# Kernel optimization log

Measured on AMD Instinct MI355X. Metric: run time of the kernel, lower is better.

## Reference

```python
import jax, jax.numpy as jnp
import numpy as np

N, E, T, F = 20000, 320000, 64, 16
HG, HT = 128, 256


def setup_inputs() -> dict:
    key = jax.random.key(0)
    ks = jax.random.split(key, 18)
    s = 0.05
    p = lambda k, shape: jax.random.normal(k, shape, jnp.float32) * s
    return {
        "x_seq": jax.random.normal(ks[0], (1, T, N, F), jnp.float32),
        "edge_index": jax.random.randint(ks[1], (2, E), 0, N, jnp.int32),
        # SAGEConv 1 (PyG default: mean aggregation; lin_l on aggregated neighbors w/ bias, lin_r on root w/o bias)
        "W1l": p(ks[2], (HG, F)), "b1l": p(ks[3], (HG,)), "W1r": p(ks[4], (HG, F)),
        # SAGEConv 2
        "W2l": p(ks[5], (HG, HG)), "b2l": p(ks[6], (HG,)), "W2r": p(ks[7], (HG, HG)),
        # GRU (torch gate order: r, z, n)
        "W_ih": p(ks[8], (3 * HT, HG)), "W_hh": p(ks[9], (3 * HT, HT)),
        "b_ih": p(ks[10], (3 * HT,)), "b_hh": p(ks[11], (3 * HT,)),
        # head: Linear(HT,64) -> ReLU -> Linear(64,1)
        "Wh1": p(ks[12], (64, HT)), "bh1": p(ks[13], (64,)),
        "Wh2": p(ks[14], (1, 64)), "bh2": p(ks[15], (1,)),
    }


def reference(x_seq, edge_index, W1l, b1l, W1r, W2l, b2l, W2r,
              W_ih, W_hh, b_ih, b_hh, Wh1, bh1, Wh2, bh2):
    n_nodes = x_seq.shape[2]
    src, dst = edge_index[0], edge_index[1]
    # in-degree for mean aggregation (0 -> output 0, matching scatter-mean)
    deg = jax.ops.segment_sum(jnp.ones(src.shape[0], x_seq.dtype), dst,
                              num_segments=n_nodes)
    inv_deg = jnp.where(deg > 0, 1.0 / deg, 0.0)[:, None]  # [N,1]

    def sage(x, Wl, bl, Wr):
        # mean over incoming neighbor messages, then linear + root linear
        agg = jax.ops.segment_sum(x[src], dst, num_segments=n_nodes) * inv_deg
        return agg @ Wl.T + bl + x @ Wr.T

    def graph_step(carry, x_t):  # x_t: [N, F]
        h = jax.nn.relu(sage(x_t, W1l, b1l, W1r))
        h = jax.nn.relu(sage(h, W2l, b2l, W2r))
        return carry, h.mean(axis=0)  # [HG]

    _, Hg = jax.lax.scan(graph_step, 0, x_seq[0])  # [T, HG]

    hidden_t = W_hh.shape[1]

    def gru_step(h, x_t):
        gi = x_t @ W_ih.T + b_ih
        gh = h @ W_hh.T + b_hh
        i_r, i_z, i_n = jnp.split(gi, 3)
        h_r, h_z, h_n = jnp.split(gh, 3)
        r = jax.nn.sigmoid(i_r + h_r)
        z = jax.nn.sigmoid(i_z + h_z)
        n = jnp.tanh(i_n + r * h_n)
        h_new = (1.0 - z) * n + z * h
        return h_new, h_new

    h0 = jnp.zeros((hidden_t,), x_seq.dtype)
    h_last, _ = jax.lax.scan(gru_step, h0, Hg)  # [HT]

    y = jax.nn.relu(h_last @ Wh1.T + bh1) @ Wh2.T + bh2  # [1]
    return y
```

## Files before the change

### kernel.cpp

```cpp
#include <hip/hip_runtime.h>
#include <hip/hip_bf16.h>

#define N_NODES 20000
#define N_EDGES 320000
#define T_STEPS 64
#define F_IN    16
#define HGd     128
#define HTd     256
#define INVN    (1.0f/20000.0f)
#define NTILES   625
#define S1T      79
#define NG64     313
#define QSCALE   64.0f
#define INVQ     (1.0f/64.0f)
#define QX       32.0f
#define INVQX    (1.0f/32.0f)

typedef __attribute__((ext_vector_type(8))) short short8;
typedef __attribute__((ext_vector_type(4))) float f32x4;
typedef __attribute__((ext_vector_type(2))) float f32x2;
typedef __attribute__((ext_vector_type(2))) _Float16 half2t;

static __device__ __forceinline__ ushort f2bf(float f) {
    __hip_bfloat16 b = __float2bfloat16(f);
    return *reinterpret_cast<ushort*>(&b);
}
static __device__ __forceinline__ half2t u2h(uint u) {
    half2t h; __builtin_memcpy(&h, &u, 4); return h;
}
static __device__ __forceinline__ uint packf16(float a, float b) {
    auto h = __builtin_amdgcn_cvt_pkrtz(a, b);
    uint u; __builtin_memcpy(&u, &h, 4); return u;
}

__global__ void k_zero(int* __restrict__ deg, float* __restrict__ HgP,
                       int* __restrict__ cnt, int* __restrict__ jobc,
                       int* __restrict__ bins) {
    int i = blockIdx.x * blockDim.x + threadIdx.x;
    if (i < N_NODES) deg[i] = 0;
    if (i < T_STEPS * 8 * HGd) HgP[i] = 0.0f;
    if (i < 2) cnt[i] = 0;
    if (i < 1024) jobc[i] = 0;
    if (i < 256) bins[i] = 0;
}

__global__ void k_degree(const int* __restrict__ ei, int* __restrict__ deg) {
    int e = blockIdx.x * blockDim.x + threadIdx.x;
    if (e < N_EDGES) atomicAdd(&deg[ei[N_EDGES + e]], 1);
}

__global__ __launch_bounds__(1024) void k_scan(const int* __restrict__ deg,
        int* __restrict__ rp, int* __restrict__ cursor, float* __restrict__ invd) {
    __shared__ int sh[1024];
    __shared__ int carry_s;
    int tid = threadIdx.x;
    if (tid == 0) { carry_s = 0; rp[0] = 0; }
    __syncthreads();
    for (int base = 0; base < N_NODES; base += 1024) {
        int i = base + tid;
        int v = (i < N_NODES) ? deg[i] : 0;
        sh[tid] = v;
        __syncthreads();
        for (int off = 1; off < 1024; off <<= 1) {
            int t = (tid >= off) ? sh[tid - off] : 0;
            __syncthreads();
            sh[tid] += t;
            __syncthreads();
        }
        int inc = sh[tid] + carry_s;
        if (i < N_NODES) {
            rp[i + 1] = inc;
            cursor[i] = inc - v;
            invd[i] = (v > 0) ? (1.0f / (float)v) : 0.0f;
        }
        __syncthreads();
        if (tid == 1023) carry_s = inc;
        __syncthreads();
    }
}

__global__ void k_fill(const int* __restrict__ ei, int* __restrict__ cursor,
                       int* __restrict__ csr) {
    int e = blockIdx.x * blockDim.x + threadIdx.x;
    if (e < N_EDGES) {
        int d = ei[N_EDGES + e];
        int p = atomicAdd(&cursor[d], 1);
        csr[p] = ei[e];
    }
}

__global__ void k_hist(const int* __restrict__ deg, int* __restrict__ bins) {
    int i = blockIdx.x * blockDim.x + threadIdx.x;
    if (i < N_NODES) atomicAdd(&bins[min(deg[i], 255)], 1);
}

__global__ __launch_bounds__(256) void k_binscan(const int* __restrict__ bins,
        int* __restrict__ bincur, int* __restrict__ nodebefore, int* __restrict__ edgebefore) {
    __shared__ int sh[256], she[256];
    int tid = threadIdx.x;
    int b = bins[tid];
    sh[tid] = b;
    she[tid] = b * tid;
    __syncthreads();
    for (int off = 1; off < 256; off <<= 1) {
        int v = (tid >= off) ? sh[tid - off] : 0;
        int ve = (tid >= off) ? she[tid - off] : 0;
        __syncthreads();
        sh[tid] += v; she[tid] += ve;
        __syncthreads();
    }
    bincur[tid] = sh[tid] - b;
    nodebefore[tid] = sh[tid] - b;
    edgebefore[tid] = she[tid] - b * tid;
}

__global__ void k_perm(const int* __restrict__ deg, int* __restrict__ bincur,
                       const int* __restrict__ nodebefore, const int* __restrict__ edgebefore,
                       const float* __restrict__ invd,
                       int* __restrict__ perm, int* __restrict__ pos,
                       int* __restrict__ rp2, float* __restrict__ invd2,
                       int* __restrict__ degs2) {
    int i = blockIdx.x * blockDim.x + threadIdx.x;
    if (i < N_NODES) {
        int d = min(deg[i], 255);
        int p = atomicAdd(&bincur[d], 1);
        int rank = p - nodebefore[d];
        perm[p] = i;
        pos[i] = p;
        rp2[p] = edgebefore[d] + rank * d;
        invd2[p] = invd[i];
        degs2[p] = deg[i];
        if (i == 0) rp2[N_NODES] = N_EDGES;
    }
}

__global__ void k_csr2(const int* __restrict__ rp, const int* __restrict__ pos,
                       const int* __restrict__ rp2, const int* __restrict__ csr,
                       int* __restrict__ csr2) {
    int i = blockIdx.x * blockDim.x + threadIdx.x;
    if (i < N_NODES) {
        int s = rp[i], e = rp[i + 1];
        int o = rp2[pos[i]];
        for (int k = s; k < e; ++k) csr2[o + (k - s)] = csr[k];
    }
}

__global__ __launch_bounds__(512) void k_tb(const int* __restrict__ rp2, int* __restrict__ tb) {
    __shared__ int sh[512];
    int t = threadIdx.x;
    int md = 0;
    if (t < NG64 && t * 64 < N_NODES) {
        int last = min((t + 1) * 64, N_NODES) - 1;
        md = rp2[last + 1] - rp2[last];
    }
    sh[t] = 64 * md;
    __syncthreads();
    for (int off = 1; off < 512; off <<= 1) {
        int v = (t >= off) ? sh[t - off] : 0;
        __syncthreads();
        sh[t] += v;
        __syncthreads();
    }
    tb[t + 1] = sh[t];
    if (t == 0) tb[0] = 0;
}

__global__ void k_csr3(const int* __restrict__ rp2, const int* __restrict__ tb,
                       const int* __restrict__ csr2, int* __restrict__ csr3) {
    int p = blockIdx.x * blockDim.x + threadIdx.x;
    if (p < N_NODES) {
        int s = rp2[p], d = rp2[p + 1] - s;
        int base = tb[p >> 6];
        int lane = p & 63;
        for (int j = 0; j < d; ++j) csr3[base + j * 64 + lane] = csr2[s + j];
    }
}

__global__ void k_qx(const float* __restrict__ xs, int* __restrict__ x8, int n4) {
    int i = blockIdx.x * blockDim.x + threadIdx.x;
    if (i < n4) {
        float4 v = reinterpret_cast<const float4*>(xs)[i];
        int q8 = __builtin_amdgcn_cvt_pk_fp8_f32(v.x * QX, v.y * QX, 0, false);
        q8 = __builtin_amdgcn_cvt_pk_fp8_f32(v.z * QX, v.w * QX, q8, true);
        x8[i] = q8;
    }
}

__global__ void k_prepw(const float* __restrict__ W1l, const float* __restrict__ W1r,
                        const float* __restrict__ W2l, const float* __restrict__ W2r,
                        const float* __restrict__ W_ih, const float* __restrict__ W_hh,
                        ushort* __restrict__ W1T2, ushort* __restrict__ WT2,
                        float* __restrict__ WihT, uint* __restrict__ W_hhq) {
    int i = blockIdx.x * blockDim.x + threadIdx.x;
    const int n1 = 128 * 32, n2 = 128 * 256, n3 = 128 * 768, n4 = 128 * 768;
    if (i < n1) {
        int o = i >> 5, k = i & 31;
        float v = (k < 16) ? W1l[o * 16 + k] : W1r[o * 16 + (k - 16)];
        W1T2[i] = f2bf(v);
    } else if (i < n1 + n2) {
        int j = i - n1; int o = j >> 8, k = j & 255;
        float v = (k < 128) ? W2l[o * 128 + k] : W2r[o * 128 + (k - 128)];
        WT2[j] = f2bf(v);
    } else if (i < n1 + n2 + n3) {
        int j = i - n1 - n2; int k = j / 768, g = j % 768;
        WihT[j] = W_ih[g * 128 + k];
    } else if (i < n1 + n2 + n3 + n4) {
        int j = i - n1 - n2 - n3; int dw = j / 768, row = j % 768;
        float a = W_hh[(size_t)row * HTd + 2 * dw];
        float b = W_hh[(size_t)row * HTd + 2 * dw + 1];
        W_hhq[j] = packf16(a, b);
    }
}

__global__ __launch_bounds__(256) void k_sage1(
        const char* __restrict__ x8_, const int* __restrict__ tb,
        const int* __restrict__ csr3, const int* __restrict__ degs2,
        const float* __restrict__ invd2,
        const ushort* __restrict__ W1T2, const float* __restrict__ b1l,
        const int* __restrict__ perm, uchar1* __restrict__ h1q_,
        int* __restrict__ jobc, int C) {
    __shared__ ushort u[256 * 40];
    __shared__ int pnode[256];
    __shared__ int job_s;
    int tid = threadIdx.x;
    int l = tid & 63, w = tid >> 6;
    int lane15 = l & 15, g4 = l >> 4;
    const int xcd = blockIdx.x & 7;
    const int cmin = (C < 8) ? C : 8;
    const int ci = xcd % cmin;
    const int reps = (C >= 8) ? (C >> 3) : 1;
    int* ctr = jobc + ci;
    const int njobs = reps * S1T;

    short8 bfr1[2];
    float bb1[2];
#pragma unroll
    for (int ct = 0; ct < 2; ++ct) {
        int o16 = w * 32 + ct * 16 + lane15;
        bfr1[ct] = *reinterpret_cast<const short8*>(W1T2 + o16 * 32 + g4 * 8);
        bb1[ct] = b1l[o16];
    }

    for (;;) {
        if (tid == 0) job_s = atomicAdd(ctr, 1);
        __syncthreads();
        int job = job_s;
        if (job >= njobs) break;
        int rep = job / S1T;
        int tile = job - rep * S1T;
        int tl = ci + (rep << 3);
        const char* xq = x8_ + (size_t)tl * N_NODES * F_IN;
        char* h1q = (char*)h1q_ + (size_t)tl * N_NODES * HGd;
        int p = tile * 256 + tid;
        int node = (p < N_NODES) ? perm[p] : -1;
        pnode[tid] = node;

        float acc[16];
#pragma unroll
        for (int k = 0; k < 16; ++k) acc[k] = 0.0f;
        float rootv[16];
#pragma unroll
        for (int k = 0; k < 16; ++k) rootv[k] = 0.0f;
        if (node >= 0) {
            int d = degs2[p];
            const int base = tb[p >> 6] + (p & 63);
            for (int j = 0; j < d; ++j) {
                int idx = csr3[base + j * 64];
                uint4 row = *reinterpret_cast<const uint4*>(xq + (size_t)idx * F_IN);
#pragma unroll
                for (int c = 0; c < 4; ++c) {
                    uint vd = c == 0 ? row.x : c == 1 ? row.y : c == 2 ? row.z : row.w;
                    f32x2 lo = __builtin_amdgcn_cvt_pk_f32_fp8((int)vd, false);
                    f32x2 hi = __builtin_amdgcn_cvt_pk_f32_fp8((int)vd, true);
                    acc[4 * c + 0] += lo.x; acc[4 * c + 1] += lo.y;
                    acc[4 * c + 2] += hi.x; acc[4 * c + 3] += hi.y;
                }
            }
            float id = invd2[p] * INVQX;
#pragma unroll
            for (int k = 0; k < 16; ++k) acc[k] *= id;
            uint4 rv = *reinterpret_cast<const uint4*>(xq + (size_t)node * F_IN);
#pragma unroll
            for (int c = 0; c < 4; ++c) {
                uint vd = c == 0 ? rv.x : c == 1 ? rv.y : c == 2 ? rv.z : rv.w;
                f32x2 lo = __builtin_amdgcn_cvt_pk_f32_fp8((int)vd, false);
                f32x2 hi = __builtin_amdgcn_cvt_pk_f32_fp8((int)vd, true);
                rootv[4 * c + 0] = lo.x * INVQX; rootv[4 * c + 1] = lo.y * INVQX;
                rootv[4 * c + 2] = hi.x * INVQX; rootv[4 * c + 3] = hi.y * INVQX;
            }
        }
        {
            uint dw[16];
#pragma unroll
            for (int i = 0; i < 8; ++i)
                dw[i] = (uint)f2bf(acc[2 * i]) | ((uint)f2bf(acc[2 * i + 1]) << 16);
#pragma unroll
            for (int i = 0; i < 8; ++i)
                dw[8 + i] = (uint)f2bf(rootv[2 * i]) | ((uint)f2bf(rootv[2 * i + 1]) << 16);
            ushort* ur = u + tid * 40;
#pragma unroll
            for (int c = 0; c < 4; ++c)
                *reinterpret_cast<uint4*>(ur + c * 8) =
                    make_uint4(dw[4 * c], dw[4 * c + 1], dw[4 * c + 2], dw[4 * c + 3]);
        }
        __syncthreads();

#pragma unroll 4
        for (int rt = 0; rt < 16; ++rt) {
            int row = rt * 16 + lane15;
            short8 af = *reinterpret_cast<const short8*>(u + row * 40 + g4 * 8);
            f32x4 a0 = __builtin_amdgcn_mfma_f32_16x16x32_bf16(af, bfr1[0], (f32x4)(0.0f), 0, 0, 0);
            f32x4 a1 = __builtin_amdgcn_mfma_f32_16x16x32_bf16(af, bfr1[1], (f32x4)(0.0f), 0, 0, 0);
#pragma unroll
            for (int j = 0; j < 4; ++j) {
                int nl = rt * 16 + g4 * 4 + j;
                int nd = pnode[nl];
                if (nd >= 0) {
                    float v0 = fmaxf(a0[j] + bb1[0], 0.0f) * QSCALE;
                    float v1 = fmaxf(a1[j] + bb1[1], 0.0f) * QSCALE;
                    int q0 = __builtin_amdgcn_cvt_pk_fp8_f32(v0, v0, 0, false);
                    int q1 = __builtin_amdgcn_cvt_pk_fp8_f32(v1, v1, 0, false);
                    h1q[(size_t)nd * HGd + w * 32 + lane15] = (char)q0;
                    h1q[(size_t)nd * HGd + w * 32 + 16 + lane15] = (char)q1;
                }
            }
        }
    }
}

__global__ __launch_bounds__(256) void k_sage2(
        const uchar1* __restrict__ h1q_,
        const int* __restrict__ rp2, const int* __restrict__ csr2,
        const float* __restrict__ invd2,
        const ushort* __restrict__ WT2, const float* __restrict__ b2l,
        const int* __restrict__ perm, float* __restrict__ HgP,
        int* __restrict__ jobc, int t0, int C) {
    __shared__ uint4 usm4[32 * 512 / 16];
    __shared__ int pnode[32];
    __shared__ int job_s;
    char* ub = (char*)usm4;
    int tid = threadIdx.x;
    int l = tid & 63, w = tid >> 6;
    int lane15 = l & 15, g4 = l >> 4;
    const int xcd = blockIdx.x & 7;
    const int cmin = (C < 8) ? C : 8;
    const int ci = xcd % cmin;
    const int reps = (C >= 8) ? (C >> 3) : 1;
    int* ctr = jobc + ci;
    const int njobs = reps * NTILES;

    short8 bfr[2][8];
    float bb[2];
#pragma unroll
    for (int ct = 0; ct < 2; ++ct) {
        int n = w * 32 + ct * 16 + lane15;
        const ushort* bp = WT2 + n * 256 + g4 * 8;
#pragma unroll
        for (int ks = 0; ks < 8; ++ks)
            bfr[ct][ks] = *reinterpret_cast<const short8*>(bp + ks * 32);
        bb[ct] = b2l[n];
    }

    for (;;) {
        if (tid == 0) job_s = atomicAdd(ctr, 1);
        __syncthreads();
        int job = job_s;
        if (job >= njobs) break;
        int rep = job / NTILES;
        int tile = job - rep * NTILES;
        int tl = ci + ((reps - 1 - rep) << 3);
        int t = t0 + tl;
        const char* h1q = (const char*)h1q_ + (size_t)tl * N_NODES * HGd;
        int nbase = tile * 32;
        if (tid < 32) pnode[tid] = perm[nbase + tid];
        __syncthreads();

        {
            int nl = tid >> 3, seg = tid & 7;
            uint4 v = *reinterpret_cast<const uint4*>(h1q + (size_t)pnode[nl] * HGd + seg * 16);
            uint bw[8];
#pragma unroll
            for (int d = 0; d < 4; ++d) {
                uint vd = d == 0 ? v.x : d == 1 ? v.y : d == 2 ? v.z : v.w;
                f32x2 plo = __builtin_amdgcn_cvt_pk_f32_fp8((int)vd, false);
                f32x2 phi = __builtin_amdgcn_cvt_pk_f32_fp8((int)vd, true);
                bw[2 * d]     = (uint)f2bf(plo.x * INVQ) | ((uint)f2bf(plo.y * INVQ) << 16);
                bw[2 * d + 1] = (uint)f2bf(phi.x * INVQ) | ((uint)f2bf(phi.y * INVQ) << 16);
            }
            int base = nl * 512 + 256 + seg * 32;
            int swz = (nl & 7) << 4;
            *reinterpret_cast<uint4*>(ub + (base ^ swz)) =
                make_uint4(bw[0], bw[1], bw[2], bw[3]);
            *reinterpret_cast<uint4*>(ub + ((base + 16) ^ swz)) =
                make_uint4(bw[4], bw[5], bw[6], bw[7]);
        }

#pragma unroll
        for (int g = 0; g < 2; ++g) {
            int nl = w * 8 + g * 4 + g4;
            int sl = rp2[nbase + nl], el = rp2[nbase + nl + 1];
            float af[8] = {0, 0, 0, 0, 0, 0, 0, 0};
            if (el > sl) {
                int idx[8];
#pragma unroll
                for (int uu = 0; uu < 8; ++uu) idx[uu] = csr2[min(sl + uu, el - 1)];
                for (int j = sl; j < el; j += 8) {
                    uint2 vv[8];
#pragma unroll
                    for (int uu = 0; uu < 8; ++uu)
                        vv[uu] = *reinterpret_cast<const uint2*>(h1q + (size_t)idx[uu] * HGd + lane15 * 8);
                    int jn = j + 8;
#pragma unroll
                    for (int uu = 0; uu < 8; ++uu) idx[uu] = csr2[min(jn + uu, el - 1)];
#pragma unroll
                    for (int uu = 0; uu < 8; ++uu) {
                        uint vx = (j + uu < el) ? vv[uu].x : 0u;
                        uint vy = (j + uu < el) ? vv[uu].y : 0u;
                        f32x2 p0 = __builtin_amdgcn_cvt_pk_f32_fp8((int)vx, false);
                        f32x2 p1 = __builtin_amdgcn_cvt_pk_f32_fp8((int)vx, true);
                        f32x2 p2 = __builtin_amdgcn_cvt_pk_f32_fp8((int)vy, false);
                        f32x2 p3 = __builtin_amdgcn_cvt_pk_f32_fp8((int)vy, true);
                        af[0] += p0.x; af[1] += p0.y; af[2] += p1.x; af[3] += p1.y;
                        af[4] += p2.x; af[5] += p2.y; af[6] += p3.x; af[7] += p3.y;
                    }
                }
            }
            float id = invd2[nbase + nl] * INVQ;
            uint4 pk;
            pk.x = (uint)f2bf(af[0] * id) | ((uint)f2bf(af[1] * id) << 16);
            pk.y = (uint)f2bf(af[2] * id) | ((uint)f2bf(af[3] * id) << 16);
            pk.z = (uint)f2bf(af[4] * id) | ((uint)f2bf(af[5] * id) << 16);
            pk.w = (uint)f2bf(af[6] * id) | ((uint)f2bf(af[7] * id) << 16);
            *reinterpret_cast<uint4*>(ub + ((nl * 512 + lane15 * 16) ^ ((nl & 7) << 4))) = pk;
        }
        __syncthreads();

        f32x4 acc[2][2];
#pragma unroll
        for (int rt = 0; rt < 2; ++rt)
#pragma unroll
            for (int ct = 0; ct < 2; ++ct) acc[rt][ct] = (f32x4)(0.0f);

#pragma unroll
        for (int ks = 0; ks < 8; ++ks) {
#pragma unroll
            for (int rt = 0; rt < 2; ++rt) {
                int row = rt * 16 + lane15;
                int byt = (row * 512 + (ks * 32 + g4 * 8) * 2) ^ ((row & 7) << 4);
                short8 af = *reinterpret_cast<const short8*>(ub + byt);
                acc[rt][0] = __builtin_amdgcn_mfma_f32_16x16x32_bf16(af, bfr[0][ks], acc[rt][0], 0, 0, 0);
                acc[rt][1] = __builtin_amdgcn_mfma_f32_16x16x32_bf16(af, bfr[1][ks], acc[rt][1], 0, 0, 0);
            }
        }

#pragma unroll
        for (int ct = 0; ct < 2; ++ct) {
            float sum = 0.f;
#pragma unroll
            for (int rt = 0; rt < 2; ++rt)
#pragma unroll
                for (int j = 0; j < 4; ++j)
                    sum += fmaxf(acc[rt][ct][j] + bb[ct], 0.f);
            sum += __shfl_xor(sum, 16);
            sum += __shfl_xor(sum, 32);
            if (g4 == 0) {
                int n = w * 32 + ct * 16 + lane15;
                atomicAdd(&HgP[(t * 8 + (job & 7)) * HGd + n], sum);
            }
        }
    }
}

__global__ __launch_bounds__(768) void k_gi(const float* __restrict__ HgP,
        const float* __restrict__ WihT, const float* __restrict__ b_ih,
        float* __restrict__ gi_all) {
    __shared__ float x[HGd];
    int t = blockIdx.x, g = threadIdx.x;
    if (g < HGd) {
        float s = 0.f;
#pragma unroll
        for (int p = 0; p < 8; ++p) s += HgP[(t * 8 + p) * HGd + g];
        x[g] = s * INVN;
    }
    __syncthreads();
    float a = b_ih[g];
    for (int k = 0; k < HGd; ++k) a += WihT[k * 768 + g] * x[k];
    gi_all[t * 768 + g] = a;
}

__global__ __launch_bounds__(768, 3) void k_gru1b(const float* __restrict__ gi_all,
        const uint* __restrict__ W_hhq, const float* __restrict__ b_hh,
        const float* __restrict__ Wh1, const float* __restrict__ bh1,
        const float* __restrict__ Wh2, const float* __restrict__ bh2,
        float* __restrict__ out) {
    int tid = threadIdx.x;
    uint wv[128];
#pragma unroll
    for (int i = 0; i < 128; ++i) wv[i] = W_hhq[i * 768 + tid];
    float bh = b_hh[tid];

    __shared__ float hs[HTd];
    __shared__ uint h2s[HTd / 2];
    __shared__ float gh[3 * HTd];
    if (tid < HTd) hs[tid] = 0.0f;
    if (tid < HTd / 2) h2s[tid] = 0u;
    __syncthreads();

    for (int t = 0; t < T_STEPS; ++t) {
        float s = bh;
#pragma unroll
        for (int i = 0; i < 128; i += 4) {
            uint4 hh = *reinterpret_cast<const uint4*>(&h2s[i]);
            s = __builtin_amdgcn_fdot2(u2h(wv[i + 0]), u2h(hh.x), s, false);
            s = __builtin_amdgcn_fdot2(u2h(wv[i + 1]), u2h(hh.y), s, false);
            s = __builtin_amdgcn_fdot2(u2h(wv[i + 2]), u2h(hh.z), s, false);
            s = __builtin_amdgcn_fdot2(u2h(wv[i + 3]), u2h(hh.w), s, false);
        }
        gh[tid] = s;
        __syncthreads();
        if (tid < HTd) {
            float gir = gi_all[t * 768 + tid];
            float giz = gi_all[t * 768 + HTd + tid];
            float gin = gi_all[t * 768 + 2 * HTd + tid];
            float r = 1.0f / (1.0f + expf(-(gir + gh[tid])));
            float z = 1.0f / (1.0f + expf(-(giz + gh[HTd + tid])));
            float n = tanhf(gin + r * gh[2 * HTd + tid]);
            hs[tid] = (1.0f - z) * n + z * hs[tid];
        }
        __syncthreads();
        if (tid < HTd / 2)
            h2s[tid] = packf16(hs[2 * tid], hs[2 * tid + 1]);
        __syncthreads();
    }

    __shared__ float act[64];
    if (tid < 64) {
        float a = bh1[tid];
        const float* wr = Wh1 + tid * HTd;
        for (int k = 0; k < HTd; k += 4) {
            float4 wv4 = *reinterpret_cast<const float4*>(wr + k);
            a += wv4.x * hs[k] + wv4.y * hs[k + 1] + wv4.z * hs[k + 2] + wv4.w * hs[k + 3];
        }
        act[tid] = fmaxf(a, 0.0f);
    }
    __syncthreads();
    if (tid == 0) {
        float y = bh2[0];
        for (int j = 0; j < 64; ++j) y += Wh2[j] * act[j];
        out[0] = y;
    }
}

extern "C" void kernel_launch(void* const* d_in, const int* in_sizes, int n_in,
                              void* d_out, int out_size, void* d_ws, size_t ws_size,
                              hipStream_t stream) {
    const float* x_seq = (const float*)d_in[0];
    const int*   ei    = (const int*)d_in[1];
    const float* W1l   = (const float*)d_in[2];
    const float* b1l   = (const float*)d_in[3];
    const float* W1r   = (const float*)d_in[4];
    const float* W2l   = (const float*)d_in[5];
    const float* b2l   = (const float*)d_in[6];
    const float* W2r   = (const float*)d_in[7];
    const float* W_ih  = (const float*)d_in[8];
    const float* W_hh  = (const float*)d_in[9];
    const float* b_ih  = (const float*)d_in[10];
    const float* b_hh  = (const float*)d_in[11];
    const float* Wh1   = (const float*)d_in[12];
    const float* bh1   = (const float*)d_in[13];
    const float* Wh2   = (const float*)d_in[14];
    const float* bh2   = (const float*)d_in[15];
    float* out = (float*)d_out;

    char* ws = (char*)d_ws;
    size_t off = 0;
    auto take = [&](size_t nbytes) -> void* {
        void* p = (void*)(ws + off);
        off += (nbytes + 255) & ~(size_t)255;
        return p;
    };
    int*    deg    = (int*)take(N_NODES * 4);
    int*    rp     = (int*)take((N_NODES + 1) * 4);
    int*    cursor = (int*)take(N_NODES * 4);
    int*    csr    = (int*)take(N_EDGES * 4);
    float*  invd   = (float*)take(N_NODES * 4);
    int*    perm   = (int*)take(N_NODES * 4);
    int*    pos    = (int*)take(N_NODES * 4);
    int*    rp2    = (int*)take((N_NODES + 2) * 4);
    int*    csr2   = (int*)take(N_EDGES * 4);
    float*  invd2  = (float*)take(N_NODES * 4);
    int*    degs2  = (int*)take(N_NODES * 4);
    int*    tb     = (int*)take(520 * 4);
    int*    csr3   = (int*)take(360000 * 4);
    int*    bins   = (int*)take(256 * 4);
    int*    bincur = (int*)take(256 * 4);
    int*    nodeb  = (int*)take(256 * 4);
    int*    edgeb  = (int*)take(256 * 4);
    ushort* W1T2   = (ushort*)take(128 * 32 * 2);
    ushort* WT2    = (ushort*)take(128 * 256 * 2);
    float*  WihT   = (float*)take(128 * 768 * 4);
    uint*   W_hhq  = (uint*)take(128 * 768 * 4);
    float*  HgP    = (float*)take(T_STEPS * 8 * HGd * 4);
    float*  gi_all = (float*)take(T_STEPS * 768 * 4);
    int*    cnt    = (int*)take(256);
    int*    jobc   = (int*)take(1024 * 4);

    const size_t slice_q = ((size_t)N_NODES * HGd + 255) & ~(size_t)255;
    const size_t slice_x = ((size_t)N_NODES * F_IN + 255) & ~(size_t)255;
    int T_CH = 64;
    while (T_CH > 1 && off + (size_t)T_CH * (slice_q + slice_x) > ws_size)
        T_CH >>= 1;
    uchar1* h1q = (uchar1*)take((size_t)T_CH * slice_q);
    char*   x8  = (char*)take((size_t)T_CH * slice_x);

    k_zero<<<256, 256, 0, stream>>>(deg, HgP, cnt, jobc, bins);
    k_degree<<<(N_EDGES + 255) / 256, 256, 0, stream>>>(ei, deg);
    k_scan<<<1, 1024, 0, stream>>>(deg, rp, cursor, invd);
    k_fill<<<(N_EDGES + 255) / 256, 256, 0, stream>>>(ei, cursor, csr);
    k_hist<<<(N_NODES + 255) / 256, 256, 0, stream>>>(deg, bins);
    k_binscan<<<1, 256, 0, stream>>>(bins, bincur, nodeb, edgeb);
    k_perm<<<(N_NODES + 255) / 256, 256, 0, stream>>>(deg, bincur, nodeb, edgeb, invd,
                                                      perm, pos, rp2, invd2, degs2);
    k_csr2<<<(N_NODES + 255) / 256, 256, 0, stream>>>(rp, pos, rp2, csr, csr2);
    k_tb<<<1, 512, 0, stream>>>(rp2, tb);
    k_csr3<<<(N_NODES + 255) / 256, 256, 0, stream>>>(rp2, tb, csr2, csr3);
    {
        int total = 128 * 32 + 128 * 256 + 128 * 768 + 128 * 768;
        k_prepw<<<(total + 255) / 256, 256, 0, stream>>>(W1l, W1r, W2l, W2r, W_ih, W_hh,
                                                         W1T2, WT2, WihT, W_hhq);
    }
    int chunk = 0;
    for (int t0 = 0; t0 < T_STEPS; t0 += T_CH, ++chunk) {
        int C = T_CH;
        int n4 = C * N_NODES * F_IN / 4;
        k_qx<<<(n4 + 255) / 256, 256, 0, stream>>>(
            x_seq + (size_t)t0 * N_NODES * F_IN, (int*)x8, n4);
        k_sage1<<<2048, 256, 0, stream>>>(x8, tb, csr3, degs2, invd2, W1T2, b1l, perm,
                                          h1q, jobc + (chunk & 1) * 16, C);
        k_sage2<<<2048, 256, 0, stream>>>(h1q, rp2, csr2, invd2, WT2, b2l, perm, HgP,
                                          jobc + (chunk & 1) * 16 + 8, t0, C);
    }
    k_gi<<<T_STEPS, 768, 0, stream>>>(HgP, WihT, b_ih, gi_all);
    k_gru1b<<<1, 768, 0, stream>>>(gi_all, W_hhq, b_hh, Wh1, bh1, Wh2, bh2, out);
}
```

Baseline: 1.059 ms.

## Store layer-1 activations as fp16 and gather with padded CSR in sage2

```diff
diff --git a/kernel.cpp b/kernel.cpp
--- a/kernel.cpp
+++ b/kernel.cpp
@@ -11,10 +11,9 @@
 #define NTILES   625
 #define S1T      79
 #define NG64     313
-#define QSCALE   64.0f
-#define INVQ     (1.0f/64.0f)
 #define QX       32.0f
 #define INVQX    (1.0f/32.0f)
+#define S_HALF   ((N_NODES + 1) * HGd)
 
 typedef __attribute__((ext_vector_type(8))) short short8;
 typedef __attribute__((ext_vector_type(4))) float f32x4;
@@ -28,20 +27,29 @@
 static __device__ __forceinline__ half2t u2h(uint u) {
     half2t h; __builtin_memcpy(&h, &u, 4); return h;
 }
+static __device__ __forceinline__ uint h2u(half2t h) {
+    uint u; __builtin_memcpy(&u, &h, 4); return u;
+}
 static __device__ __forceinline__ uint packf16(float a, float b) {
     auto h = __builtin_amdgcn_cvt_pkrtz(a, b);
     uint u; __builtin_memcpy(&u, &h, 4); return u;
 }
+static __device__ __forceinline__ ushort f2h(float a) {
+    return (ushort)(packf16(a, a) & 0xffffu);
+}
 
 __global__ void k_zero(int* __restrict__ deg, float* __restrict__ HgP,
-                       int* __restrict__ cnt, int* __restrict__ jobc,
-                       int* __restrict__ bins) {
+                       int* __restrict__ jobc, int* __restrict__ bins,
+                       uint* __restrict__ h1f, int tch) {
     int i = blockIdx.x * blockDim.x + threadIdx.x;
     if (i < N_NODES) deg[i] = 0;
     if (i < T_STEPS * 8 * HGd) HgP[i] = 0.0f;
-    if (i < 2) cnt[i] = 0;
     if (i < 1024) jobc[i] = 0;
     if (i < 256) bins[i] = 0;
+    if (i < tch * 64) {
+        int sl = i >> 6, j = i & 63;
+        h1f[(size_t)sl * (S_HALF / 2) + (size_t)N_NODES * (HGd / 2) + j] = 0u;
+    }
 }
 
 __global__ void k_degree(const int* __restrict__ ei, int* __restrict__ deg) {
@@ -95,31 +103,37 @@
 }
 
 __global__ __launch_bounds__(256) void k_binscan(const int* __restrict__ bins,
-        int* __restrict__ bincur, int* __restrict__ nodebefore, int* __restrict__ edgebefore) {
-    __shared__ int sh[256], she[256];
+        int* __restrict__ bincur, int* __restrict__ nodebefore,
+        int* __restrict__ edgebefore, int* __restrict__ edgebp, int* __restrict__ rp2p) {
+    __shared__ int sh[256], she[256], shp[256];
     int tid = threadIdx.x;
     int b = bins[tid];
+    int dp = (tid + 7) & ~7;
     sh[tid] = b;
     she[tid] = b * tid;
+    shp[tid] = b * dp;
     __syncthreads();
     for (int off = 1; off < 256; off <<= 1) {
         int v = (tid >= off) ? sh[tid - off] : 0;
         int ve = (tid >= off) ? she[tid - off] : 0;
-        __syncthreads();
-        sh[tid] += v; she[tid] += ve;
+        int vp = (tid >= off) ? shp[tid - off] : 0;
+        __syncthreads();
+        sh[tid] += v; she[tid] += ve; shp[tid] += vp;
         __syncthreads();
     }
     bincur[tid] = sh[tid] - b;
     nodebefore[tid] = sh[tid] - b;
     edgebefore[tid] = she[tid] - b * tid;
+    edgebp[tid] = shp[tid] - b * dp;
+    if (tid == 255) rp2p[N_NODES] = shp[255];
 }
 
 __global__ void k_perm(const int* __restrict__ deg, int* __restrict__ bincur,
                        const int* __restrict__ nodebefore, const int* __restrict__ edgebefore,
-                       const float* __restrict__ invd,
+                       const int* __restrict__ edgebp, const float* __restrict__ invd,
                        int* __restrict__ perm, int* __restrict__ pos,
                        int* __restrict__ rp2, float* __restrict__ invd2,
-                       int* __restrict__ degs2) {
+                       int* __restrict__ degs2, int* __restrict__ rp2p) {
     int i = blockIdx.x * blockDim.x + threadIdx.x;
     if (i < N_NODES) {
         int d = min(deg[i], 255);
@@ -128,6 +142,7 @@
         perm[p] = i;
         pos[i] = p;
         rp2[p] = edgebefore[d] + rank * d;
+        rp2p[p] = edgebp[d] + rank * ((d + 7) & ~7);
         invd2[p] = invd[i];
         degs2[p] = deg[i];
         if (i == 0) rp2[N_NODES] = N_EDGES;
@@ -145,6 +160,19 @@
     }
 }
 
+__global__ void k_csr2p(const int* __restrict__ rp, const int* __restrict__ pos,
+                        const int* __restrict__ rp2p, const int* __restrict__ csr,
+                        int* __restrict__ csr2p) {
+    int i = blockIdx.x * blockDim.x + threadIdx.x;
+    if (i < N_NODES) {
+        int s = rp[i], d = rp[i + 1] - s;
+        int dp = (d + 7) & ~7;
+        int o = rp2p[pos[i]];
+        for (int k = 0; k < d; ++k) csr2p[o + k] = csr[s + k];
+        for (int k = d; k < dp; ++k) csr2p[o + k] = N_NODES;
+    }
+}
+
 __global__ __launch_bounds__(512) void k_tb(const int* __restrict__ rp2, int* __restrict__ tb) {
     __shared__ int sh[512];
     int t = threadIdx.x;
@@ -189,7 +217,7 @@
 __global__ void k_prepw(const float* __restrict__ W1l, const float* __restrict__ W1r,
                         const float* __restrict__ W2l, const float* __restrict__ W2r,
                         const float* __restrict__ W_ih, const float* __restrict__ W_hh,
-                        ushort* __restrict__ W1T2, ushort* __restrict__ WT2,
+                        ushort* __restrict__ W1T2, ushort* __restrict__ WT2f,
                         float* __restrict__ WihT, uint* __restrict__ W_hhq) {
     int i = blockIdx.x * blockDim.x + threadIdx.x;
     const int n1 = 128 * 32, n2 = 128 * 256, n3 = 128 * 768, n4 = 128 * 768;
@@ -200,7 +228,7 @@
     } else if (i < n1 + n2) {
         int j = i - n1; int o = j >> 8, k = j & 255;
         float v = (k < 128) ? W2l[o * 128 + k] : W2r[o * 128 + (k - 128)];
-        WT2[j] = f2bf(v);
+        WT2f[j] = f2h(v);
     } else if (i < n1 + n2 + n3) {
         int j = i - n1 - n2; int k = j / 768, g = j % 768;
         WihT[j] = W_ih[g * 128 + k];
@@ -217,7 +245,7 @@
         const int* __restrict__ csr3, const int* __restrict__ degs2,
         const float* __restrict__ invd2,
         const ushort* __restrict__ W1T2, const float* __restrict__ b1l,
-        const int* __restrict__ perm, uchar1* __restrict__ h1q_,
+        const int* __restrict__ perm, ushort* __restrict__ h1f_,
         int* __restrict__ jobc, int C) {
     __shared__ ushort u[256 * 40];
     __shared__ int pnode[256];
@@ -250,7 +278,7 @@
         int tile = job - rep * S1T;
         int tl = ci + (rep << 3);
         const char* xq = x8_ + (size_t)tl * N_NODES * F_IN;
-        char* h1q = (char*)h1q_ + (size_t)tl * N_NODES * HGd;
+        ushort* h1f = h1f_ + (size_t)tl * S_HALF;
         int p = tile * 256 + tid;
         int node = (p < N_NODES) ? perm[p] : -1;
         pnode[tid] = node;
@@ -316,12 +344,10 @@
                 int nl = rt * 16 + g4 * 4 + j;
                 int nd = pnode[nl];
                 if (nd >= 0) {
-                    float v0 = fmaxf(a0[j] + bb1[0], 0.0f) * QSCALE;
-                    float v1 = fmaxf(a1[j] + bb1[1], 0.0f) * QSCALE;
-                    int q0 = __builtin_amdgcn_cvt_pk_fp8_f32(v0, v0, 0, false);
-                    int q1 = __builtin_amdgcn_cvt_pk_fp8_f32(v1, v1, 0, false);
-                    h1q[(size_t)nd * HGd + w * 32 + lane15] = (char)q0;
-                    h1q[(size_t)nd * HGd + w * 32 + 16 + lane15] = (char)q1;
+                    float v0 = fmaxf(a0[j] + bb1[0], 0.0f);
+                    float v1 = fmaxf(a1[j] + bb1[1], 0.0f);
+                    h1f[(size_t)nd * HGd + w * 32 + lane15] = f2h(v0);
+                    h1f[(size_t)nd * HGd + w * 32 + 16 + lane15] = f2h(v1);
                 }
             }
         }
@@ -329,10 +355,10 @@
 }
 
 __global__ __launch_bounds__(256) void k_sage2(
-        const uchar1* __restrict__ h1q_,
-        const int* __restrict__ rp2, const int* __restrict__ csr2,
+        const ushort* __restrict__ h1f_,
+        const int* __restrict__ rp2p, const int* __restrict__ csr2p,
         const float* __restrict__ invd2,
-        const ushort* __restrict__ WT2, const float* __restrict__ b2l,
+        const ushort* __restrict__ WT2f, const float* __restrict__ b2l,
         const int* __restrict__ perm, float* __restrict__ HgP,
         int* __restrict__ jobc, int t0, int C) {
     __shared__ uint4 usm4[32 * 512 / 16];
@@ -354,7 +380,7 @@
 #pragma unroll
     for (int ct = 0; ct < 2; ++ct) {
         int n = w * 32 + ct * 16 + lane15;
-        const ushort* bp = WT2 + n * 256 + g4 * 8;
+        const ushort* bp = WT2f + n * 256 + g4 * 8;
 #pragma unroll
         for (int ks = 0; ks < 8; ++ks)
             bfr[ct][ks] = *reinterpret_cast<const short8*>(bp + ks * 32);
@@ -370,67 +396,53 @@
         int tile = job - rep * NTILES;
         int tl = ci + ((reps - 1 - rep) << 3);
         int t = t0 + tl;
-        const char* h1q = (const char*)h1q_ + (size_t)tl * N_NODES * HGd;
+        const ushort* h1f = h1f_ + (size_t)tl * S_HALF;
         int nbase = tile * 32;
         if (tid < 32) pnode[tid] = perm[nbase + tid];
         __syncthreads();
 
-        {
-            int nl = tid >> 3, seg = tid & 7;
-            uint4 v = *reinterpret_cast<const uint4*>(h1q + (size_t)pnode[nl] * HGd + seg * 16);
-            uint bw[8];
-#pragma unroll
-            for (int d = 0; d < 4; ++d) {
-                uint vd = d == 0 ? v.x : d == 1 ? v.y : d == 2 ? v.z : v.w;
-                f32x2 plo = __builtin_amdgcn_cvt_pk_f32_fp8((int)vd, false);
-                f32x2 phi = __builtin_amdgcn_cvt_pk_f32_fp8((int)vd, true);
-                bw[2 * d]     = (uint)f2bf(plo.x * INVQ) | ((uint)f2bf(plo.y * INVQ) << 16);
-                bw[2 * d + 1] = (uint)f2bf(phi.x * INVQ) | ((uint)f2bf(phi.y * INVQ) << 16);
-            }
-            int base = nl * 512 + 256 + seg * 32;
-            int swz = (nl & 7) << 4;
-            *reinterpret_cast<uint4*>(ub + (base ^ swz)) =
-                make_uint4(bw[0], bw[1], bw[2], bw[3]);
-            *reinterpret_cast<uint4*>(ub + ((base + 16) ^ swz)) =
-                make_uint4(bw[4], bw[5], bw[6], bw[7]);
+        for (int i = tid; i < 512; i += 256) {
+            int nl = i >> 4, seg = i & 15;
+            uint4 v = *reinterpret_cast<const uint4*>(h1f + (size_t)pnode[nl] * HGd + seg * 8);
+            *reinterpret_cast<uint4*>(ub + ((nl * 1024 / 2 + 256 + seg * 16) ^ ((nl & 7) << 4))) = v;
         }
 
 #pragma unroll
         for (int g = 0; g < 2; ++g) {
             int nl = w * 8 + g * 4 + g4;
-            int sl = rp2[nbase + nl], el = rp2[nbase + nl + 1];
-            float af[8] = {0, 0, 0, 0, 0, 0, 0, 0};
-            if (el > sl) {
+            int sl = rp2p[nbase + nl];
+            int dp = rp2p[nbase + nl + 1] - sl;
+            const int* cp = csr2p + sl;
+            half2t a0 = (half2t)0, a1 = (half2t)0, a2 = (half2t)0, a3 = (half2t)0;
+            if (dp > 0) {
                 int idx[8];
 #pragma unroll
-                for (int uu = 0; uu < 8; ++uu) idx[uu] = csr2[min(sl + uu, el - 1)];
-                for (int j = sl; j < el; j += 8) {
-                    uint2 vv[8];
+                for (int uu = 0; uu < 8; ++uu) idx[uu] = cp[uu];
+                for (int j = 0; j < dp; j += 8) {
+                    uint4 vv[8];
 #pragma unroll
                     for (int uu = 0; uu < 8; ++uu)
-                        vv[uu] = *reinterpret_cast<const uint2*>(h1q + (size_t)idx[uu] * HGd + lane15 * 8);
-                    int jn = j + 8;
-#pragma unroll
-                    for (int uu = 0; uu < 8; ++uu) idx[uu] = csr2[min(jn + uu, el - 1)];
+                        vv[uu] = *reinterpret_cast<const uint4*>(h1f + (size_t)idx[uu] * HGd + lane15 * 8);
+                    cp += 8;
+#pragma unroll
+                    for (int uu = 0; uu < 8; ++uu) idx[uu] = cp[uu];
 #pragma unroll
                     for (int uu = 0; uu < 8; ++uu) {
-                        uint vx = (j + uu < el) ? vv[uu].x : 0u;
-                        uint vy = (j + uu < el) ? vv[uu].y : 0u;
-                        f32x2 p0 = __builtin_amdgcn_cvt_pk_f32_fp8((int)vx, false);
-                        f32x2 p1 = __builtin_amdgcn_cvt_pk_f32_fp8((int)vx, true);
-                        f32x2 p2 = __builtin_amdgcn_cvt_pk_f32_fp8((int)vy, false);
-                        f32x2 p3 = __builtin_amdgcn_cvt_pk_f32_fp8((int)vy, true);
-                        af[0] += p0.x; af[1] += p0.y; af[2] += p1.x; af[3] += p1.y;
-                        af[4] += p2.x; af[5] += p2.y; af[6] += p3.x; af[7] += p3.y;
+                        a0 += u2h(vv[uu].x);
+                        a1 += u2h(vv[uu].y);
+                        a2 += u2h(vv[uu].z);
+                        a3 += u2h(vv[uu].w);
                     }
                 }
             }
-            float id = invd2[nbase + nl] * INVQ;
+            float id = invd2[nbase + nl];
+            _Float16 idh = (_Float16)id;
+            half2t idv; idv[0] = idh; idv[1] = idh;
             uint4 pk;
-            pk.x = (uint)f2bf(af[0] * id) | ((uint)f2bf(af[1] * id) << 16);
-            pk.y = (uint)f2bf(af[2] * id) | ((uint)f2bf(af[3] * id) << 16);
-            pk.z = (uint)f2bf(af[4] * id) | ((uint)f2bf(af[5] * id) << 16);
-            pk.w = (uint)f2bf(af[6] * id) | ((uint)f2bf(af[7] * id) << 16);
+            pk.x = h2u(a0 * idv);
+            pk.y = h2u(a1 * idv);
+            pk.z = h2u(a2 * idv);
+            pk.w = h2u(a3 * idv);
             *reinterpret_cast<uint4*>(ub + ((nl * 512 + lane15 * 16) ^ ((nl & 7) << 4))) = pk;
         }
         __syncthreads();
@@ -448,8 +460,8 @@
                 int row = rt * 16 + lane15;
                 int byt = (row * 512 + (ks * 32 + g4 * 8) * 2) ^ ((row & 7) << 4);
                 short8 af = *reinterpret_cast<const short8*>(ub + byt);
-                acc[rt][0] = __builtin_amdgcn_mfma_f32_16x16x32_bf16(af, bfr[0][ks], acc[rt][0], 0, 0, 0);
-                acc[rt][1] = __builtin_amdgcn_mfma_f32_16x16x32_bf16(af, bfr[1][ks], acc[rt][1], 0, 0, 0);
+                acc[rt][0] = __builtin_amdgcn_mfma_f32_16x16x32_f16(af, bfr[0][ks], acc[rt][0], 0, 0, 0);
+                acc[rt][1] = __builtin_amdgcn_mfma_f32_16x16x32_f16(af, bfr[1][ks], acc[rt][1], 0, 0, 0);
             }
         }
 
@@ -587,7 +599,9 @@
     int*    perm   = (int*)take(N_NODES * 4);
     int*    pos    = (int*)take(N_NODES * 4);
     int*    rp2    = (int*)take((N_NODES + 2) * 4);
+    int*    rp2p   = (int*)take((N_NODES + 2) * 4);
     int*    csr2   = (int*)take(N_EDGES * 4);
+    int*    csr2p  = (int*)take(480100 * 4);
     float*  invd2  = (float*)take(N_NODES * 4);
     int*    degs2  = (int*)take(N_NODES * 4);
     int*    tb     = (int*)take(520 * 4);
@@ -596,38 +610,39 @@
     int*    bincur = (int*)take(256 * 4);
     int*    nodeb  = (int*)take(256 * 4);
     int*    edgeb  = (int*)take(256 * 4);
+    int*    edgebp = (int*)take(256 * 4);
     ushort* W1T2   = (ushort*)take(128 * 32 * 2);
-    ushort* WT2    = (ushort*)take(128 * 256 * 2);
+    ushort* WT2f   = (ushort*)take(128 * 256 * 2);
     float*  WihT   = (float*)take(128 * 768 * 4);
     uint*   W_hhq  = (uint*)take(128 * 768 * 4);
     float*  HgP    = (float*)take(T_STEPS * 8 * HGd * 4);
     float*  gi_all = (float*)take(T_STEPS * 768 * 4);
-    int*    cnt    = (int*)take(256);
     int*    jobc   = (int*)take(1024 * 4);
 
-    const size_t slice_q = ((size_t)N_NODES * HGd + 255) & ~(size_t)255;
+    const size_t slice_h = (size_t)S_HALF * 2;
     const size_t slice_x = ((size_t)N_NODES * F_IN + 255) & ~(size_t)255;
     int T_CH = 64;
-    while (T_CH > 1 && off + (size_t)T_CH * (slice_q + slice_x) > ws_size)
+    while (T_CH > 1 && off + (size_t)T_CH * (slice_h + slice_x) > ws_size)
         T_CH >>= 1;
-    uchar1* h1q = (uchar1*)take((size_t)T_CH * slice_q);
+    ushort* h1f = (ushort*)take((size_t)T_CH * slice_h);
     char*   x8  = (char*)take((size_t)T_CH * slice_x);
 
-    k_zero<<<256, 256, 0, stream>>>(deg, HgP, cnt, jobc, bins);
+    k_zero<<<256, 256, 0, stream>>>(deg, HgP, jobc, bins, (uint*)h1f, T_CH);
     k_degree<<<(N_EDGES + 255) / 256, 256, 0, stream>>>(ei, deg);
     k_scan<<<1, 1024, 0, stream>>>(deg, rp, cursor, invd);
     k_fill<<<(N_EDGES + 255) / 256, 256, 0, stream>>>(ei, cursor, csr);
     k_hist<<<(N_NODES + 255) / 256, 256, 0, stream>>>(deg, bins);
-    k_binscan<<<1, 256, 0, stream>>>(bins, bincur, nodeb, edgeb);
-    k_perm<<<(N_NODES + 255) / 256, 256, 0, stream>>>(deg, bincur, nodeb, edgeb, invd,
-                                                      perm, pos, rp2, invd2, degs2);
+    k_binscan<<<1, 256, 0, stream>>>(bins, bincur, nodeb, edgeb, edgebp, rp2p);
+    k_perm<<<(N_NODES + 255) / 256, 256, 0, stream>>>(deg, bincur, nodeb, edgeb, edgebp,
+                                                      invd, perm, pos, rp2, invd2, degs2, rp2p);
     k_csr2<<<(N_NODES + 255) / 256, 256, 0, stream>>>(rp, pos, rp2, csr, csr2);
+    k_csr2p<<<(N_NODES + 255) / 256, 256, 0, stream>>>(rp, pos, rp2p, csr, csr2p);
     k_tb<<<1, 512, 0, stream>>>(rp2, tb);
     k_csr3<<<(N_NODES + 255) / 256, 256, 0, stream>>>(rp2, tb, csr2, csr3);
     {
         int total = 128 * 32 + 128 * 256 + 128 * 768 + 128 * 768;
         k_prepw<<<(total + 255) / 256, 256, 0, stream>>>(W1l, W1r, W2l, W2r, W_ih, W_hh,
-                                                         W1T2, WT2, WihT, W_hhq);
+                                                         W1T2, WT2f, WihT, W_hhq);
     }
     int chunk = 0;
     for (int t0 = 0; t0 < T_STEPS; t0 += T_CH, ++chunk) {
@@ -636,9 +651,9 @@
         k_qx<<<(n4 + 255) / 256, 256, 0, stream>>>(
             x_seq + (size_t)t0 * N_NODES * F_IN, (int*)x8, n4);
         k_sage1<<<2048, 256, 0, stream>>>(x8, tb, csr3, degs2, invd2, W1T2, b1l, perm,
-                                          h1q, jobc + (chunk & 1) * 16, C);
-        k_sage2<<<2048, 256, 0, stream>>>(h1q, rp2, csr2, invd2, WT2, b2l, perm, HgP,
-                                          jobc + (chunk & 1) * 16 + 8, t0, C);
+                                          h1f, jobc + chunk * 16, C);
+        k_sage2<<<2048, 256, 0, stream>>>(h1f, rp2p, csr2p, invd2, WT2f, b2l, perm, HgP,
+                                          jobc + chunk * 16 + 8, t0, C);
     }
     k_gi<<<T_STEPS, 768, 0, stream>>>(HgP, WihT, b_ih, gi_all);
     k_gru1b<<<1, 768, 0, stream>>>(gi_all, W_hhq, b_hh, Wh1, bh1, Wh2, bh2, out);
```

Result: slower. 1.123 ms (+6.0%).
